# Kernel tuning notes

Measured on AMD Instinct MI355X. Metric: run time of the kernel, lower is better.

The kernel has to match this reference:

```python
import jax, jax.numpy as jnp
import numpy as np

B, T = 32, 64
I, O, H = 64, 64, 512
N, W = 128, 64           # memory slots, slot width
IF = 3 * W + 6           # interface size


def setup_inputs() -> dict:
    key = jax.random.key(0)
    ks = jax.random.split(key, 6)
    s = 0.05
    return {
        "x": jax.random.normal(ks[0], (B, T, I), jnp.float32),
        "W_ih": jax.random.normal(ks[1], (4 * H, I + W), jnp.float32) * s,
        "W_hh": jax.random.normal(ks[2], (4 * H, H), jnp.float32) * s,
        "b_ih": jnp.zeros((4 * H,), jnp.float32),
        "b_hh": jnp.zeros((4 * H,), jnp.float32),
        "W_if": jax.random.normal(ks[3], (IF, H), jnp.float32) * s,
        "b_if": jnp.zeros((IF,), jnp.float32),
        "W_out": jax.random.normal(ks[4], (O, H + W), jnp.float32) * s,
        "b_out": jnp.zeros((O,), jnp.float32),
    }


def reference(x, W_ih, W_hh, b_ih, b_hh, W_if, b_if, W_out, b_out):
    Bb, Tt, _ = x.shape
    dt = x.dtype
    eye = jnp.eye(N, dtype=dt)
    batch_idx = jnp.arange(Bb)[:, None]

    def step(carry, x_t):
        h, c, mem, usage, prec, link, rw, rvec = carry
        # --- LSTM controller (PyTorch gate order i,f,g,o) ---
        inp = jnp.concatenate([x_t, rvec], axis=-1)
        gates = inp @ W_ih.T + h @ W_hh.T + b_ih + b_hh
        i_g, f_g, g_g, o_g = jnp.split(gates, 4, axis=-1)
        c = jax.nn.sigmoid(f_g) * c + jax.nn.sigmoid(i_g) * jnp.tanh(g_g)
        h = jax.nn.sigmoid(o_g) * jnp.tanh(c)
        itf = h @ W_if.T + b_if
        # --- parse interface ---
        erase = jax.nn.sigmoid(itf[:, :W])
        wvec = itf[:, W:2 * W]
        wg = jax.nn.sigmoid(itf[:, 2 * W])
        ag = jax.nn.sigmoid(itf[:, 2 * W + 1])
        rstr = jnp.log1p(jnp.exp(itf[:, 3 * W + 2]))  # softplus
        # --- allocation weighting (sort usage asc, shifted cumprod, scatter) ---
        idx = jnp.argsort(usage, axis=-1)
        usage_sorted = jnp.take_along_axis(usage, idx, axis=-1)
        cprod = jnp.cumprod(usage_sorted, axis=-1)
        cprod = jnp.concatenate([jnp.ones((Bb, 1), dt), cprod[:, :-1]], axis=-1)
        alloc_in_order = (1.0 - usage_sorted) * cprod
        alloc = jnp.zeros_like(usage).at[batch_idx, idx].set(alloc_in_order)
        ww = wg[:, None] * ag[:, None] * alloc  # [B,N]
        # --- erase + add write ---
        mem = mem * (1.0 - ww[:, :, None] * erase[:, None, :]) + ww[:, :, None] * wvec[:, None, :]
        usage = usage + (1.0 - usage) * ww
        # --- temporal link / precedence ---
        ww_ij = ww[:, :, None] + ww[:, None, :]
        link = (1.0 - ww_ij) * link + prec[:, :, None] * ww[:, None, :]
        link = link * (1.0 - eye)
        prec = (1.0 - ww.sum(-1, keepdims=True)) * prec + ww
        # --- read weights (NOTE: source uses itf[:, :W] as read key) ---
        rmode = jax.nn.softmax(itf[:, -3:], axis=-1)
        rkey = itf[:, :W]
        dot = jnp.einsum('bw,bnw->bn', rkey, mem)
        kn = jnp.linalg.norm(rkey, axis=-1, keepdims=True) + 1e-8
        mn = jnp.linalg.norm(mem, axis=-1) + 1e-8
        cw = jax.nn.softmax(dot / (kn * mn) * rstr[:, None], axis=-1)
        bw = jnp.einsum('bnm,bn->bm', link, rw)   # link^T @ rw
        fw = jnp.einsum('bnm,bm->bn', link, rw)   # link @ rw
        wts = rmode[:, 0:1] * bw + rmode[:, 1:2] * fw + rmode[:, 2:3] * cw + 1e-8
        wts = wts / wts.sum(-1, keepdims=True)
        rvec = jnp.einsum('bn,bnw->bw', wts, mem)
        out = jnp.concatenate([h, rvec], axis=-1) @ W_out.T + b_out
        return (h, c, mem, usage, prec, link, wts, rvec), out

    z = lambda *s: jnp.zeros(s, dt)
    carry0 = (z(Bb, H), z(Bb, H), z(Bb, N, W), z(Bb, N), z(Bb, N), z(Bb, N, N), z(Bb, N), z(Bb, W))
    _, outs = jax.lax.scan(step, carry0, jnp.swapaxes(x, 0, 1))
    return jnp.swapaxes(outs, 0, 1)  # [B,T,O]
```

## Files before the change

### kernel.cpp

```cpp
#include <hip/hip_runtime.h>
#include <math.h>

#define Bb 32
#define Tt 64
#define Ii 64
#define Oo 64
#define Hh 512
#define Nn 128
#define Wd 64
#define IFs 198
#define KV 640
#define G4 2048

#define NP1 128
#define NWG 160
#define NT 512

#define P2_MEM    0
#define P2_H      8320
#define P2_SCR    8896
#define P2_ITF    10944
#define P2_ERASE  11168
#define P2_WVEC   11232
#define P2_USAGE  11296
#define P2_PREC   11424
#define P2_RW     11552
#define P2_WW     11680
#define P2_SCAN   11808
#define P2_SS     11936
#define P2_SCAL   12064
#define P2_BIF    12080
#define P2_ALLOC  12304
#define P1_WIF    0
#define P1_BS     13464
#define P1_V      13720
#define P1_CC     15016
#define P1_HSL    15144
#define P1_PACC   15272
#define SMEM_FLOATS 23592
#define SMEM_BYTES (SMEM_FLOATS * 4)

#define S_WWSUM 0

__device__ __align__(16) float g_WT[KV * G4];
__device__ __align__(16) float g_bsum[G4];
typedef unsigned long long u64;
__device__ u64 g_h64[2 * Bb * Hh];
__device__ u64 g_rv64[Bb * Wd];
__device__ u64 g_if64[Bb * 8 * 200];

__device__ __forceinline__ float sigf(float v) { return 1.f / (1.f + expf(-v)); }

__device__ __forceinline__ u64 ldrelax(const u64* p) {
  return __hip_atomic_load(p, __ATOMIC_RELAXED, __HIP_MEMORY_SCOPE_AGENT);
}
__device__ __forceinline__ void tstore(u64* p, unsigned tag, float v) {
  u64 val = ((u64)tag << 32) | (u64)__float_as_uint(v);
  __hip_atomic_store(p, val, __ATOMIC_RELAXED, __HIP_MEMORY_SCOPE_AGENT);
}
__device__ __forceinline__ float fixwait(const u64* p, u64 v, unsigned tag) {
  while ((unsigned)(v >> 32) != tag) {
    __builtin_amdgcn_s_sleep(1);
    v = ldrelax(p);
  }
  return __uint_as_float((unsigned)(v & 0xffffffffu));
}

#define TIN 512
__global__ __launch_bounds__(TIN) void dnc_init(const float* __restrict__ W_ih,
                                                const float* __restrict__ W_hh,
                                                const float* __restrict__ b_ih,
                                                const float* __restrict__ b_hh) {
  __shared__ float tile[64][65];
  const int tid = threadIdx.x;
  int i0 = blockIdx.x * blockDim.x + tid;
  int st = gridDim.x * blockDim.x;
  for (int idx = i0; idx < G4; idx += st) g_bsum[idx] = b_ih[idx] + b_hh[idx];
  for (int idx = i0; idx < 2 * Bb * Hh; idx += st) g_h64[idx] = 0ull;
  for (int idx = i0; idx < Bb * Wd; idx += st) g_rv64[idx] = 0ull;
  for (int idx = i0; idx < Bb * 8 * 200; idx += st) g_if64[idx] = 0ull;

  for (int tileId = blockIdx.x; tileId < 320; tileId += gridDim.x) {
    int tc = tileId >> 5, tj = tileId & 31;
    for (int k = tid; k < 64 * 64; k += TIN) {
      int r = k >> 6, cl = k & 63;
      int j = tj * 64 + r, c = tc * 64 + cl;
      tile[r][cl] = (c < 128) ? W_ih[j * 128 + c] : W_hh[j * 512 + (c - 128)];
    }
    __syncthreads();
    for (int k = tid; k < 64 * 64; k += TIN) {
      int cl = k >> 6, rjj = k & 63;
      int c = tc * 64 + cl;
      int rp = (c < 128) ? (512 + c) : (c - 128);
      g_WT[(size_t)rp * G4 + tj * 64 + rjj] = tile[rjj][cl];
    }
    __syncthreads();
  }
}

__global__ __launch_bounds__(NT) void dnc_main(const float* __restrict__ x,
                                               const float* __restrict__ W_if,
                                               const float* __restrict__ b_if,
                                               const float* __restrict__ W_out,
                                               const float* __restrict__ b_out,
                                               float* __restrict__ out) {
  extern __shared__ float sm[];
  const int tid = threadIdx.x;
  const int wg = blockIdx.x;

  if (wg < NP1) {
    const int jb = wg & 7;
    const int bb = wg >> 3;
    const int b0 = bb * 2;
    for (int i = tid; i < IFs * 64; i += NT) {
      int o = i >> 6, c = i & 63;
      sm[P1_WIF + o * 68 + c] = W_if[(size_t)o * Hh + jb * 64 + c];
    }
    if (tid < 64) {
      int gq = tid >> 4, m = tid & 15;
      ((float4*)(sm + P1_BS))[tid] = ((const float4*)g_bsum)[gq * 128 + jb * 16 + m];
    }
    if (tid < 128) sm[P1_CC + tid] = 0.f;
    __syncthreads();

    for (int t = 0; t < Tt; ++t) {
      {
        const u64* hsrc = g_h64 + (size_t)((t + 1) & 1) * (Bb * Hh);
        const int u = tid;
        const u64* a0 = hsrc + (size_t)b0 * Hh + u;
        const u64* a1 = hsrc + (size_t)(b0 + 1) * Hh + u;
        u64 v0 = ldrelax(a0), v1 = ldrelax(a1);
        float2 hh;
        hh.x = fixwait(a0, v0, (unsigned)t);
        hh.y = fixwait(a1, v1, (unsigned)t);
        *(float2*)(sm + P1_V + u * 2) = hh;
        if (tid < 128) {
          const int bl2 = tid >> 6, i = tid & 63;
          float xv = x[((size_t)(b0 + bl2) * Tt + t) * Ii + i];
          sm[P1_V + (512 + i) * 2 + bl2] = xv;
        }
      }
      __syncthreads();

      {
        const int fg = tid & 31, ks = tid >> 5;
        const int fcolA = ((fg >> 4) * 128) + jb * 16 + (fg & 15);
        const float* v2 = sm + P1_V + ks * 80;
        const float4* wpA = (const float4*)g_WT + (size_t)(ks * 40) * 512 + fcolA;
        if (ks >= 14) {
          const int j = tid & 63;
          const u64* r0 = g_rv64 + (size_t)b0 * Wd + j;
          const u64* r1 = g_rv64 + (size_t)(b0 + 1) * Wd + j;
          u64 u0 = ldrelax(r0), u1 = ldrelax(r1);
          float2 rv;
          rv.x = fixwait(r0, u0, (unsigned)t);
          rv.y = fixwait(r1, u1, (unsigned)t);
          *(float2*)(sm + P1_V + (576 + j) * 2) = rv;
        }
        float4 aA0 = {0.f, 0.f, 0.f, 0.f}, aA1 = {0.f, 0.f, 0.f, 0.f};
        float4 aB0 = {0.f, 0.f, 0.f, 0.f}, aB1 = {0.f, 0.f, 0.f, 0.f};
#pragma unroll 4
        for (int r = 0; r < 40; ++r) {
          float4 wA = wpA[(size_t)r * 512];
          float4 wB = wpA[(size_t)r * 512 + 256];
          float2 vv = *(const float2*)(v2 + r * 2);
          aA0.x += wA.x * vv.x; aA0.y += wA.y * vv.x; aA0.z += wA.z * vv.x; aA0.w += wA.w * vv.x;
          aA1.x += wA.x * vv.y; aA1.y += wA.y * vv.y; aA1.z += wA.z * vv.y; aA1.w += wA.w * vv.y;
          aB0.x += wB.x * vv.x; aB0.y += wB.y * vv.x; aB0.z += wB.z * vv.x; aB0.w += wB.w * vv.x;
          aB1.x += wB.x * vv.y; aB1.y += wB.y * vv.y; aB1.z += wB.z * vv.y; aB1.w += wB.w * vv.y;
        }
        float4* pacc = (float4*)(sm + P1_PACC);
        pacc[(ks * 2 + 0) * 65 + fg] = aA0;
        pacc[(ks * 2 + 1) * 65 + fg] = aA1;
        pacc[(ks * 2 + 0) * 65 + fg + 32] = aB0;
        pacc[(ks * 2 + 1) * 65 + fg + 32] = aB1;
      }
      __syncthreads();
      if (tid < 128) {
        const int bl = tid >> 6, l = tid & 63;
        const float* pb = sm + P1_PACC + bl * 260 + l;
        float gv0 = 0.f, gv1 = 0.f, gv2 = 0.f, gv3 = 0.f;
#pragma unroll
        for (int ks = 0; ks < 16; ++ks) {
          const float* pk = pb + ks * 520;
          gv0 += pk[0];
          gv1 += pk[64];
          gv2 += pk[128];
          gv3 += pk[192];
        }
        float ig = gv0 + sm[P1_BS + l];
        float fg = gv1 + sm[P1_BS + 64 + l];
        float gg = gv2 + sm[P1_BS + 128 + l];
        float og = gv3 + sm[P1_BS + 192 + l];
        float co = sm[P1_CC + bl * 64 + l];
        float cn = sigf(fg) * co + sigf(ig) * tanhf(gg);
        float hn = sigf(og) * tanhf(cn);
        sm[P1_CC + bl * 64 + l] = cn;
        sm[P1_HSL + bl * 64 + l] = hn;
        tstore(g_h64 + (size_t)(t & 1) * (Bb * Hh) + (size_t)(b0 + bl) * Hh + jb * 64 + l,
               (unsigned)(t + 1), hn);
      }
      __syncthreads();
      if (tid < 2 * IFs) {
        const int o = tid >> 1, bl = tid & 1;
        const float4* wr = (const float4*)(sm + P1_WIF + o * 68);
        const float4* h4 = (const float4*)(sm + P1_HSL + bl * 64);
        float acc = 0.f;
#pragma unroll 8
        for (int c4 = 0; c4 < 16; ++c4) {
          float4 w = wr[c4]; float4 h = h4[c4];
          acc += w.x * h.x + w.y * h.y + w.z * h.z + w.w * h.w;
        }
        tstore(g_if64 + ((size_t)(b0 + bl) * 8 + jb) * 200 + o, (unsigned)(t + 1), acc);
      }
    }
  } else {
    const int b = wg - NP1;
    float* SCR = sm + P2_SCR;
    float regL[32], regLT[32];
#pragma unroll
    for (int k = 0; k < 32; ++k) { regL[k] = 0.f; regLT[k] = 0.f; }
    for (int i = tid; i < Nn * 65; i += NT) sm[P2_MEM + i] = 0.f;
    if (tid < 128) { sm[P2_USAGE + tid] = 0.f; sm[P2_PREC + tid] = 0.f; sm[P2_RW + tid] = 0.f; }
    if (tid < IFs) sm[P2_BIF + tid] = b_if[tid];
    __syncthreads();
    if (tid < 64) {
      const int li = tid, i0 = 2 * li, i1 = i0 + 1;
      float u0 = sm[P2_USAGE + i0], u1 = sm[P2_USAGE + i1];
      int r0 = 0, r1 = 0;
      for (int jc = 0; jc < 32; ++jc) {
        float4 uj4 = *(const float4*)(sm + P2_USAGE + jc * 4);
#pragma unroll
        for (int e = 0; e < 4; ++e) {
          float uj = (&uj4.x)[e];
          int j = jc * 4 + e;
          r0 += (uj < u0 || (uj == u0 && j < i0)) ? 1 : 0;
          r1 += (uj < u1 || (uj == u1 && j < i1)) ? 1 : 0;
        }
      }
      sm[P2_SS + r0] = u0;
      sm[P2_SS + r1] = u1;
      float s0 = sm[P2_SS + i0], s1 = sm[P2_SS + i1];
      float p = s0 * s1;
#pragma unroll
      for (int off = 1; off < 64; off <<= 1) {
        float v = __shfl_up(p, off, 64);
        if (li >= off) p *= v;
      }
      float E = __shfl_up(p, 1, 64);
      if (li == 0) E = 1.f;
      sm[P2_SCAN + i0] = E * s0;
      sm[P2_SCAN + i1] = E * s0 * s1;
      float ex0 = (r0 > 0) ? sm[P2_SCAN + r0 - 1] : 1.f;
      float ex1 = (r1 > 0) ? sm[P2_SCAN + r1 - 1] : 1.f;
      sm[P2_ALLOC + i0] = (1.f - u0) * ex0;
      sm[P2_ALLOC + i1] = (1.f - u1) * ex1;
    }
    __syncthreads();

    for (int t = 0; t < Tt; ++t) {
      if (tid < 2 * IFs) {
        const int o = tid >> 1, hf = tid & 1;
        const u64* src = g_if64 + ((size_t)b * 8 + hf * 4) * 200 + o;
        u64 a0 = ldrelax(src), a1 = ldrelax(src + 200),
            a2 = ldrelax(src + 400), a3 = ldrelax(src + 600);
        float s = fixwait(src, a0, (unsigned)(t + 1))
                + fixwait(src + 200, a1, (unsigned)(t + 1))
                + fixwait(src + 400, a2, (unsigned)(t + 1))
                + fixwait(src + 600, a3, (unsigned)(t + 1));
        s += __shfl_xor(s, 1, 64);
        if (hf == 0) sm[P2_ITF + o] = s + sm[P2_BIF + o];
      }
      __syncthreads();
      float kn_r = 0.f, rstr_r = 0.f, rm0_r = 0.f, rm1_r = 0.f, rm2_r = 0.f;
      if (tid < 64) {
        const int li = tid, i0 = 2 * li, i1 = i0 + 1;
        float wgag = sigf(sm[P2_ITF + 128]) * sigf(sm[P2_ITF + 129]);
        float rs = sm[P2_ITF + 194];
        rstr_r = (rs > 20.f) ? rs : log1pf(expf(rs));
        float m0 = sm[P2_ITF + 195], m1 = sm[P2_ITF + 196], m2 = sm[P2_ITF + 197];
        float mx = fmaxf(m0, fmaxf(m1, m2));
        float e0 = expf(m0 - mx), e1 = expf(m1 - mx), e2 = expf(m2 - mx);
        float es = e0 + e1 + e2;
        rm0_r = e0 / es; rm1_r = e1 / es; rm2_r = e2 / es;
        float rk = sm[P2_ITF + li];
        sm[P2_ERASE + li] = sigf(rk);
        sm[P2_WVEC + li] = sm[P2_ITF + 64 + li];
        float sq = rk * rk;
#pragma unroll
        for (int off = 32; off > 0; off >>= 1) sq += __shfl_xor(sq, off, 64);
        kn_r = sqrtf(sq) + 1e-8f;
        float u0 = sm[P2_USAGE + i0], u1 = sm[P2_USAGE + i1];
        float w0 = wgag * sm[P2_ALLOC + i0];
        float w1 = wgag * sm[P2_ALLOC + i1];
        sm[P2_WW + i0] = w0; sm[P2_WW + i1] = w1;
        sm[P2_USAGE + i0] = u0 + (1.f - u0) * w0;
        sm[P2_USAGE + i1] = u1 + (1.f - u1) * w1;
        float wws = w0 + w1;
#pragma unroll
        for (int off = 32; off > 0; off >>= 1) wws += __shfl_xor(wws, off, 64);
        if (li == 0) sm[P2_SCAL + S_WWSUM] = wws;
      }
      __syncthreads();
      {
        const int n = tid & 127, ws = tid >> 7;
        float4 er[4], wv[4], kf[4];
#pragma unroll
        for (int r = 0; r < 4; ++r) {
          er[r] = *(const float4*)(sm + P2_ERASE + ws * 16 + r * 4);
          wv[r] = *(const float4*)(sm + P2_WVEC + ws * 16 + r * 4);
          kf[r] = *(const float4*)(sm + P2_ITF + ws * 16 + r * 4);
        }
        float wwn = sm[P2_WW + n];
        float dotp = 0.f, mnp = 0.f;
        const int base = P2_MEM + n * 65 + ws * 16;
#pragma unroll
        for (int q = 0; q < 16; ++q) {
          float m = sm[base + q];
          float ee = (&er[q >> 2].x)[q & 3];
          float vv = (&wv[q >> 2].x)[q & 3];
          float kk = (&kf[q >> 2].x)[q & 3];
          m = m * (1.f - wwn * ee) + wwn * vv;
          sm[base + q] = m;
          dotp += kk * m;
          mnp += m * m;
        }
        SCR[ws * 128 + n] = dotp;
        SCR[512 + ws * 128 + n] = mnp;
        const int m = n, ns = ws;
        float wwm = wwn;
        float prn = sm[P2_PREC + m];
        float bwp = 0.f, fwp = 0.f;
#pragma unroll
        for (int kq = 0; kq < 8; ++kq) {
          float4 ww4 = *(const float4*)(sm + P2_WW + ns * 32 + kq * 4);
          float4 pr4 = *(const float4*)(sm + P2_PREC + ns * 32 + kq * 4);
          float4 rw4 = *(const float4*)(sm + P2_RW + ns * 32 + kq * 4);
#pragma unroll
          for (int e = 0; e < 4; ++e) {
            int k = kq * 4 + e;
            int nn = ns * 32 + k;
            float wwo = (&ww4.x)[e];
            float pro = (&pr4.x)[e];
            float rwo = (&rw4.x)[e];
            float L = regL[k];
            L = (1.f - wwo - wwm) * L + pro * wwm;
            if (nn == m) L = 0.f;
            regL[k] = L;
            bwp += L * rwo;
            float LT = regLT[k];
            LT = (1.f - wwm - wwo) * LT + prn * wwo;
            if (nn == m) LT = 0.f;
            regLT[k] = LT;
            fwp += LT * rwo;
          }
        }
        SCR[1024 + ns * 128 + m] = bwp;
        SCR[1536 + ns * 128 + m] = fwp;
      }
      __syncthreads();
      if (tid < 64) {
        int i0 = 2 * tid, i1 = i0 + 1;
        float d0 = SCR[i0] + SCR[128 + i0] + SCR[256 + i0] + SCR[384 + i0];
        float d1 = SCR[i1] + SCR[128 + i1] + SCR[256 + i1] + SCR[384 + i1];
        float mn0 = sqrtf(SCR[512 + i0] + SCR[640 + i0] + SCR[768 + i0] + SCR[896 + i0]) + 1e-8f;
        float mn1 = sqrtf(SCR[512 + i1] + SCR[640 + i1] + SCR[768 + i1] + SCR[896 + i1]) + 1e-8f;
        float bw0 = SCR[1024 + i0] + SCR[1152 + i0] + SCR[1280 + i0] + SCR[1408 + i0];
        float bw1 = SCR[1024 + i1] + SCR[1152 + i1] + SCR[1280 + i1] + SCR[1408 + i1];
        float fw0 = SCR[1536 + i0] + SCR[1664 + i0] + SCR[1792 + i0] + SCR[1920 + i0];
        float fw1 = SCR[1536 + i1] + SCR[1664 + i1] + SCR[1792 + i1] + SCR[1920 + i1];
        float q0 = d0 / (kn_r * mn0) * rstr_r;
        float q1 = d1 / (kn_r * mn1) * rstr_r;
        float mx = fmaxf(q0, q1);
#pragma unroll
        for (int off = 32; off > 0; off >>= 1) mx = fmaxf(mx, __shfl_xor(mx, off, 64));
        float e0 = expf(q0 - mx), e1 = expf(q1 - mx);
        float es = e0 + e1;
#pragma unroll
        for (int off = 32; off > 0; off >>= 1) es += __shfl_xor(es, off, 64);
        float wv0 = rm0_r * bw0 + rm1_r * fw0 + rm2_r * (e0 / es) + 1e-8f;
        float wv1 = rm0_r * bw1 + rm1_r * fw1 + rm2_r * (e1 / es) + 1e-8f;
        float wsum = wv0 + wv1;
#pragma unroll
        for (int off = 32; off > 0; off >>= 1) wsum += __shfl_xor(wsum, off, 64);
        sm[P2_RW + i0] = wv0 / wsum;
        sm[P2_RW + i1] = wv1 / wsum;
      }
      __syncthreads();
      {
        const int w = tid & 63, ns8 = tid >> 6;
        float4 rw4[4];
#pragma unroll
        for (int r = 0; r < 4; ++r)
          rw4[r] = *(const float4*)(sm + P2_RW + ns8 * 16 + r * 4);
        float p = 0.f;
#pragma unroll
        for (int k = 0; k < 16; ++k)
          p += (&rw4[k >> 2].x)[k & 3] * sm[P2_MEM + (ns8 * 16 + k) * 65 + w];
        SCR[ns8 * 64 + w] = p;
      }
      __syncthreads();
      if (tid < 64) {
        float r = 0.f;
#pragma unroll
        for (int s2 = 0; s2 < 8; ++s2) r += SCR[s2 * 64 + tid];
        sm[P2_H + 512 + tid] = r;
        tstore(g_rv64 + (size_t)b * Wd + tid, (unsigned)(t + 1), r);
      } else if (tid < 320) {
        const int idx = tid - 64;
        const u64* hsrc = g_h64 + (size_t)(t & 1) * (Bb * Hh) + (size_t)b * Hh;
        const u64* a0 = hsrc + idx * 2;
        const u64* a1 = hsrc + idx * 2 + 1;
        u64 v0 = ldrelax(a0), v1 = ldrelax(a1);
        sm[P2_H + idx * 2] = fixwait(a0, v0, (unsigned)(t + 1));
        sm[P2_H + idx * 2 + 1] = fixwait(a1, v1, (unsigned)(t + 1));
      } else if (tid < 384) {
        const int li = tid - 320, i0 = 2 * li, i1 = i0 + 1;
        float u0 = sm[P2_USAGE + i0], u1 = sm[P2_USAGE + i1];
        int r0 = 0, r1 = 0;
        for (int jc = 0; jc < 32; ++jc) {
          float4 uj4 = *(const float4*)(sm + P2_USAGE + jc * 4);
#pragma unroll
          for (int e = 0; e < 4; ++e) {
            float uj = (&uj4.x)[e];
            int j = jc * 4 + e;
            r0 += (uj < u0 || (uj == u0 && j < i0)) ? 1 : 0;
            r1 += (uj < u1 || (uj == u1 && j < i1)) ? 1 : 0;
          }
        }
        sm[P2_SS + r0] = u0;
        sm[P2_SS + r1] = u1;
        float s0 = sm[P2_SS + i0], s1 = sm[P2_SS + i1];
        float p = s0 * s1;
#pragma unroll
        for (int off = 1; off < 64; off <<= 1) {
          float v = __shfl_up(p, off, 64);
          if (li >= off) p *= v;
        }
        float E = __shfl_up(p, 1, 64);
        if (li == 0) E = 1.f;
        sm[P2_SCAN + i0] = E * s0;
        sm[P2_SCAN + i1] = E * s0 * s1;
        float ex0 = (r0 > 0) ? sm[P2_SCAN + r0 - 1] : 1.f;
        float ex1 = (r1 > 0) ? sm[P2_SCAN + r1 - 1] : 1.f;
        sm[P2_ALLOC + i0] = (1.f - u0) * ex0;
        sm[P2_ALLOC + i1] = (1.f - u1) * ex1;
      } else {
        const int n = tid - 384;
        float wws = sm[P2_SCAL + S_WWSUM];
        sm[P2_PREC + n] = (1.f - wws) * sm[P2_PREC + n] + sm[P2_WW + n];
      }
      __syncthreads();
      {
        const int o = tid >> 3, seg = tid & 7;
        const float4* wrow = (const float4*)(W_out + (size_t)o * 576) + seg * 18;
        const float4* hb = (const float4*)(sm + P2_H) + seg * 18;
        float p = 0.f;
#pragma unroll
        for (int q = 0; q < 18; ++q) {
          float4 w = wrow[q]; float4 h = hb[q];
          p += w.x * h.x + w.y * h.y + w.z * h.z + w.w * h.w;
        }
        p += __shfl_down(p, 4, 8);
        p += __shfl_down(p, 2, 8);
        p += __shfl_down(p, 1, 8);
        if (seg == 0) out[((size_t)b * Tt + t) * Oo + o] = p + b_out[o];
      }
    }
  }
}

extern "C" void kernel_launch(void* const* d_in, const int* in_sizes, int n_in,
                              void* d_out, int out_size, void* d_ws, size_t ws_size,
                              hipStream_t stream) {
  (void)in_sizes; (void)n_in; (void)d_ws; (void)ws_size; (void)out_size;
  const float* x    = (const float*)d_in[0];
  const float* W_ih = (const float*)d_in[1];
  const float* W_hh = (const float*)d_in[2];
  const float* b_ih = (const float*)d_in[3];
  const float* b_hh = (const float*)d_in[4];
  const float* W_if = (const float*)d_in[5];
  const float* b_if = (const float*)d_in[6];
  const float* W_out = (const float*)d_in[7];
  const float* b_out = (const float*)d_in[8];
  float* out = (float*)d_out;

  dnc_init<<<320, TIN, 0, stream>>>(W_ih, W_hh, b_ih, b_hh);

  hipFuncSetAttribute((const void*)dnc_main,
                      hipFuncAttributeMaxDynamicSharedMemorySize, SMEM_BYTES);

  void* args[] = {(void*)&x, (void*)&W_if, (void*)&b_if,
                  (void*)&W_out, (void*)&b_out, (void*)&out};
  hipLaunchCooperativeKernel((void*)dnc_main, dim3(NWG), dim3(NT), args,
                             SMEM_BYTES, stream);
}
```

Measured before the change: 873.5 us.

## Remove per-step barriers by folding interface parsing and read vector into fewer phases

Eliminates the separate interface-parsing phase by computing erase in the itf-gather step and deriving write weights on the fly from double-buffered alloc and a precomputed alloc sum. The content-weight normalisation now runs redundantly in every wave and feeds the read-vector reduction through shuffles, which drops two more barriers and the separate summation phase. The usage update moves into the sort phase. Fewer __syncthreads per timestep on the serial recurrence, at the cost of some redundant transcendental and norm work per wave.

```diff
diff --git a/kernel.cpp b/kernel.cpp
--- a/kernel.cpp
+++ b/kernel.cpp
@@ -21,16 +21,14 @@
 #define P2_SCR    8896
 #define P2_ITF    10944
 #define P2_ERASE  11168
-#define P2_WVEC   11232
-#define P2_USAGE  11296
-#define P2_PREC   11424
-#define P2_RW     11552
-#define P2_WW     11680
-#define P2_SCAN   11808
-#define P2_SS     11936
-#define P2_SCAL   12064
-#define P2_BIF    12080
-#define P2_ALLOC  12304
+#define P2_USAGE  11232
+#define P2_PREC   11360
+#define P2_RW     11488
+#define P2_SCAN   11616
+#define P2_SS     11744
+#define P2_SCAL   11872
+#define P2_BIF    11888
+#define P2_ALLOC  12112
 #define P1_WIF    0
 #define P1_BS     13464
 #define P1_V      13720
@@ -39,8 +37,6 @@
 #define P1_PACC   15272
 #define SMEM_FLOATS 23592
 #define SMEM_BYTES (SMEM_FLOATS * 4)
-
-#define S_WWSUM 0
 
 __device__ __align__(16) float g_WT[KV * G4];
 __device__ __align__(16) float g_bsum[G4];
@@ -253,8 +249,14 @@
       sm[P2_SCAN + i1] = E * s0 * s1;
       float ex0 = (r0 > 0) ? sm[P2_SCAN + r0 - 1] : 1.f;
       float ex1 = (r1 > 0) ? sm[P2_SCAN + r1 - 1] : 1.f;
-      sm[P2_ALLOC + i0] = (1.f - u0) * ex0;
-      sm[P2_ALLOC + i1] = (1.f - u1) * ex1;
+      float a0 = (1.f - u0) * ex0;
+      float a1 = (1.f - u1) * ex1;
+      sm[P2_ALLOC + i0] = a0;
+      sm[P2_ALLOC + i1] = a1;
+      float as = a0 + a1;
+#pragma unroll
+      for (int off = 32; off > 0; off >>= 1) as += __shfl_xor(as, off, 64);
+      if (li == 0) sm[P2_SCAL + 0] = as;
     }
     __syncthreads();
 
@@ -269,49 +271,25 @@
                 + fixwait(src + 400, a2, (unsigned)(t + 1))
                 + fixwait(src + 600, a3, (unsigned)(t + 1));
         s += __shfl_xor(s, 1, 64);
-        if (hf == 0) sm[P2_ITF + o] = s + sm[P2_BIF + o];
-      }
-      __syncthreads();
-      float kn_r = 0.f, rstr_r = 0.f, rm0_r = 0.f, rm1_r = 0.f, rm2_r = 0.f;
-      if (tid < 64) {
-        const int li = tid, i0 = 2 * li, i1 = i0 + 1;
-        float wgag = sigf(sm[P2_ITF + 128]) * sigf(sm[P2_ITF + 129]);
-        float rs = sm[P2_ITF + 194];
-        rstr_r = (rs > 20.f) ? rs : log1pf(expf(rs));
-        float m0 = sm[P2_ITF + 195], m1 = sm[P2_ITF + 196], m2 = sm[P2_ITF + 197];
-        float mx = fmaxf(m0, fmaxf(m1, m2));
-        float e0 = expf(m0 - mx), e1 = expf(m1 - mx), e2 = expf(m2 - mx);
-        float es = e0 + e1 + e2;
-        rm0_r = e0 / es; rm1_r = e1 / es; rm2_r = e2 / es;
-        float rk = sm[P2_ITF + li];
-        sm[P2_ERASE + li] = sigf(rk);
-        sm[P2_WVEC + li] = sm[P2_ITF + 64 + li];
-        float sq = rk * rk;
-#pragma unroll
-        for (int off = 32; off > 0; off >>= 1) sq += __shfl_xor(sq, off, 64);
-        kn_r = sqrtf(sq) + 1e-8f;
-        float u0 = sm[P2_USAGE + i0], u1 = sm[P2_USAGE + i1];
-        float w0 = wgag * sm[P2_ALLOC + i0];
-        float w1 = wgag * sm[P2_ALLOC + i1];
-        sm[P2_WW + i0] = w0; sm[P2_WW + i1] = w1;
-        sm[P2_USAGE + i0] = u0 + (1.f - u0) * w0;
-        sm[P2_USAGE + i1] = u1 + (1.f - u1) * w1;
-        float wws = w0 + w1;
-#pragma unroll
-        for (int off = 32; off > 0; off >>= 1) wws += __shfl_xor(wws, off, 64);
-        if (li == 0) sm[P2_SCAL + S_WWSUM] = wws;
+        if (hf == 0) {
+          float v = s + sm[P2_BIF + o];
+          sm[P2_ITF + o] = v;
+          if (o < 64) sm[P2_ERASE + o] = sigf(v);
+        }
       }
       __syncthreads();
       {
         const int n = tid & 127, ws = tid >> 7;
+        const float* ALo = sm + P2_ALLOC + (t & 1) * 128;
+        const float wgag = sigf(sm[P2_ITF + 128]) * sigf(sm[P2_ITF + 129]);
         float4 er[4], wv[4], kf[4];
 #pragma unroll
         for (int r = 0; r < 4; ++r) {
           er[r] = *(const float4*)(sm + P2_ERASE + ws * 16 + r * 4);
-          wv[r] = *(const float4*)(sm + P2_WVEC + ws * 16 + r * 4);
+          wv[r] = *(const float4*)(sm + P2_ITF + 64 + ws * 16 + r * 4);
           kf[r] = *(const float4*)(sm + P2_ITF + ws * 16 + r * 4);
         }
-        float wwn = sm[P2_WW + n];
+        float wwn = wgag * ALo[n];
         float dotp = 0.f, mnp = 0.f;
         const int base = P2_MEM + n * 65 + ws * 16;
 #pragma unroll
@@ -333,14 +311,14 @@
         float bwp = 0.f, fwp = 0.f;
 #pragma unroll
         for (int kq = 0; kq < 8; ++kq) {
-          float4 ww4 = *(const float4*)(sm + P2_WW + ns * 32 + kq * 4);
+          float4 al4 = *(const float4*)(ALo + ns * 32 + kq * 4);
           float4 pr4 = *(const float4*)(sm + P2_PREC + ns * 32 + kq * 4);
           float4 rw4 = *(const float4*)(sm + P2_RW + ns * 32 + kq * 4);
 #pragma unroll
           for (int e = 0; e < 4; ++e) {
             int k = kq * 4 + e;
             int nn = ns * 32 + k;
-            float wwo = (&ww4.x)[e];
+            float wwo = wgag * (&al4.x)[e];
             float pro = (&pr4.x)[e];
             float rwo = (&rw4.x)[e];
             float L = regL[k];
@@ -359,8 +337,23 @@
         SCR[1536 + ns * 128 + m] = fwp;
       }
       __syncthreads();
-      if (tid < 64) {
-        int i0 = 2 * tid, i1 = i0 + 1;
+      {
+        const int l = tid & 63, wv8 = tid >> 6;
+        float rs = sm[P2_ITF + 194];
+        float rstr = (rs > 20.f) ? rs : log1pf(expf(rs));
+        float m0 = sm[P2_ITF + 195], m1 = sm[P2_ITF + 196], m2 = sm[P2_ITF + 197];
+        float mxm = fmaxf(m0, fmaxf(m1, m2));
+        float e0m = expf(m0 - mxm), e1m = expf(m1 - mxm), e2m = expf(m2 - mxm);
+        float esm = e0m + e1m + e2m;
+        float rm0 = e0m / esm, rm1 = e1m / esm, rm2 = e2m / esm;
+        float sq = 0.f;
+#pragma unroll
+        for (int c4 = 0; c4 < 16; ++c4) {
+          float4 k4 = *(const float4*)(sm + P2_ITF + c4 * 4);
+          sq += k4.x * k4.x + k4.y * k4.y + k4.z * k4.z + k4.w * k4.w;
+        }
+        float kn = sqrtf(sq) + 1e-8f;
+        const int i0 = 2 * l, i1 = i0 + 1;
         float d0 = SCR[i0] + SCR[128 + i0] + SCR[256 + i0] + SCR[384 + i0];
         float d1 = SCR[i1] + SCR[128 + i1] + SCR[256 + i1] + SCR[384 + i1];
         float mn0 = sqrtf(SCR[512 + i0] + SCR[640 + i0] + SCR[768 + i0] + SCR[896 + i0]) + 1e-8f;
@@ -369,8 +362,8 @@
         float bw1 = SCR[1024 + i1] + SCR[1152 + i1] + SCR[1280 + i1] + SCR[1408 + i1];
         float fw0 = SCR[1536 + i0] + SCR[1664 + i0] + SCR[1792 + i0] + SCR[1920 + i0];
         float fw1 = SCR[1536 + i1] + SCR[1664 + i1] + SCR[1792 + i1] + SCR[1920 + i1];
-        float q0 = d0 / (kn_r * mn0) * rstr_r;
-        float q1 = d1 / (kn_r * mn1) * rstr_r;
+        float q0 = d0 / (kn * mn0) * rstr;
+        float q1 = d1 / (kn * mn1) * rstr;
         float mx = fmaxf(q0, q1);
 #pragma unroll
         for (int off = 32; off > 0; off >>= 1) mx = fmaxf(mx, __shfl_xor(mx, off, 64));
@@ -378,45 +371,46 @@
         float es = e0 + e1;
 #pragma unroll
         for (int off = 32; off > 0; off >>= 1) es += __shfl_xor(es, off, 64);
-        float wv0 = rm0_r * bw0 + rm1_r * fw0 + rm2_r * (e0 / es) + 1e-8f;
-        float wv1 = rm0_r * bw1 + rm1_r * fw1 + rm2_r * (e1 / es) + 1e-8f;
+        float wv0 = rm0 * bw0 + rm1 * fw0 + rm2 * (e0 / es) + 1e-8f;
+        float wv1 = rm0 * bw1 + rm1 * fw1 + rm2 * (e1 / es) + 1e-8f;
         float wsum = wv0 + wv1;
 #pragma unroll
         for (int off = 32; off > 0; off >>= 1) wsum += __shfl_xor(wsum, off, 64);
-        sm[P2_RW + i0] = wv0 / wsum;
-        sm[P2_RW + i1] = wv1 / wsum;
-      }
-      __syncthreads();
-      {
-        const int w = tid & 63, ns8 = tid >> 6;
-        float4 rw4[4];
-#pragma unroll
-        for (int r = 0; r < 4; ++r)
-          rw4[r] = *(const float4*)(sm + P2_RW + ns8 * 16 + r * 4);
+        float rw0 = wv0 / wsum, rw1 = wv1 / wsum;
+        if (wv8 == 0) { sm[P2_RW + i0] = rw0; sm[P2_RW + i1] = rw1; }
+        const int w = wv8 * 8 + (l >> 3), n0 = (l & 7) * 16;
         float p = 0.f;
 #pragma unroll
-        for (int k = 0; k < 16; ++k)
-          p += (&rw4[k >> 2].x)[k & 3] * sm[P2_MEM + (ns8 * 16 + k) * 65 + w];
-        SCR[ns8 * 64 + w] = p;
-      }
-      __syncthreads();
-      if (tid < 64) {
-        float r = 0.f;
-#pragma unroll
-        for (int s2 = 0; s2 < 8; ++s2) r += SCR[s2 * 64 + tid];
-        sm[P2_H + 512 + tid] = r;
-        tstore(g_rv64 + (size_t)b * Wd + tid, (unsigned)(t + 1), r);
+        for (int k = 0; k < 16; ++k) {
+          int src = (l & 7) * 8 + (k >> 1);
+          float rwk = (k & 1) ? __shfl(rw1, src, 64) : __shfl(rw0, src, 64);
+          p += rwk * sm[P2_MEM + (n0 + k) * 65 + w];
+        }
+        p += __shfl_down(p, 4, 8);
+        p += __shfl_down(p, 2, 8);
+        p += __shfl_down(p, 1, 8);
+        if ((l & 7) == 0) {
+          tstore(g_rv64 + (size_t)b * Wd + w, (unsigned)(t + 1), p);
+          sm[P2_H + 512 + w] = p;
+        }
+      }
+      __syncthreads();
+      if (tid < 256) {
+        const u64* hsrc = g_h64 + (size_t)(t & 1) * (Bb * Hh) + (size_t)b * Hh;
+        const u64* a0 = hsrc + tid * 2;
+        const u64* a1 = hsrc + tid * 2 + 1;
+        u64 v0 = ldrelax(a0), v1 = ldrelax(a1);
+        sm[P2_H + tid * 2] = fixwait(a0, v0, (unsigned)(t + 1));
+        sm[P2_H + tid * 2 + 1] = fixwait(a1, v1, (unsigned)(t + 1));
       } else if (tid < 320) {
-        const int idx = tid - 64;
-        const u64* hsrc = g_h64 + (size_t)(t & 1) * (Bb * Hh) + (size_t)b * Hh;
-        const u64* a0 = hsrc + idx * 2;
-        const u64* a1 = hsrc + idx * 2 + 1;
-        u64 v0 = ldrelax(a0), v1 = ldrelax(a1);
-        sm[P2_H + idx * 2] = fixwait(a0, v0, (unsigned)(t + 1));
-        sm[P2_H + idx * 2 + 1] = fixwait(a1, v1, (unsigned)(t + 1));
-      } else if (tid < 384) {
-        const int li = tid - 320, i0 = 2 * li, i1 = i0 + 1;
-        float u0 = sm[P2_USAGE + i0], u1 = sm[P2_USAGE + i1];
+        const int li = tid - 256, i0 = 2 * li, i1 = i0 + 1;
+        const float* ALo = sm + P2_ALLOC + (t & 1) * 128;
+        float wgag = sigf(sm[P2_ITF + 128]) * sigf(sm[P2_ITF + 129]);
+        float u0o = sm[P2_USAGE + i0], u1o = sm[P2_USAGE + i1];
+        float u0 = u0o + (1.f - u0o) * (wgag * ALo[i0]);
+        float u1 = u1o + (1.f - u1o) * (wgag * ALo[i1]);
+        sm[P2_USAGE + i0] = u0;
+        sm[P2_USAGE + i1] = u1;
         int r0 = 0, r1 = 0;
         for (int jc = 0; jc < 32; ++jc) {
           float4 uj4 = *(const float4*)(sm + P2_USAGE + jc * 4);
@@ -443,12 +437,21 @@
         sm[P2_SCAN + i1] = E * s0 * s1;
         float ex0 = (r0 > 0) ? sm[P2_SCAN + r0 - 1] : 1.f;
         float ex1 = (r1 > 0) ? sm[P2_SCAN + r1 - 1] : 1.f;
-        sm[P2_ALLOC + i0] = (1.f - u0) * ex0;
-        sm[P2_ALLOC + i1] = (1.f - u1) * ex1;
-      } else {
-        const int n = tid - 384;
-        float wws = sm[P2_SCAL + S_WWSUM];
-        sm[P2_PREC + n] = (1.f - wws) * sm[P2_PREC + n] + sm[P2_WW + n];
+        float a0 = (1.f - u0) * ex0;
+        float a1 = (1.f - u1) * ex1;
+        float* ALn = sm + P2_ALLOC + ((t + 1) & 1) * 128;
+        ALn[i0] = a0;
+        ALn[i1] = a1;
+        float as = a0 + a1;
+#pragma unroll
+        for (int off = 32; off > 0; off >>= 1) as += __shfl_xor(as, off, 64);
+        if (li == 0) sm[P2_SCAL + ((t + 1) & 1)] = as;
+      } else if (tid < 448) {
+        const int n = tid - 320;
+        float wgag = sigf(sm[P2_ITF + 128]) * sigf(sm[P2_ITF + 129]);
+        float wws = wgag * sm[P2_SCAL + (t & 1)];
+        sm[P2_PREC + n] = (1.f - wws) * sm[P2_PREC + n]
+                        + wgag * sm[P2_ALLOC + (t & 1) * 128 + n];
       }
       __syncthreads();
       {
```

Result: slower. 960.6 us (+10.0%).
